# Kernel optimization log

Measured on AMD Instinct MI355X. Metric: run time of the kernel, lower is better.

Reference implementation:

```python
import jax, jax.numpy as jnp
import numpy as np

BINS = 64

def _soft_histogram(x, bins=BINS):
    # x: (B, C, H, W), values expected in [0, 1]
    B, C, H, W = x.shape
    x_flat = x.reshape(B, C, H * W)                       # (B, C, N)
    bin_width = 1.0 / bins
    centers = jnp.linspace(bin_width / 2, 1 - bin_width / 2, bins,
                           dtype=x.dtype)                 # (bins,)
    sigma = bin_width
    # weights: (B, C, N, bins) gaussian kernel around each bin center
    diff = x_flat[..., None] - centers                    # (B, C, N, bins)
    weights = jnp.exp(-(diff ** 2) / (2.0 * sigma ** 2))
    hist = weights.sum(axis=2)                            # (B, C, bins)
    hist = hist / (hist.sum(axis=-1, keepdims=True) + 1e-08)
    return hist


def setup_inputs() -> dict:
    key = jax.random.key(0)
    k1, k2 = jax.random.split(key)
    pred = jax.random.uniform(k1, (4, 3, 512, 512), dtype=jnp.float32)
    target = jax.random.uniform(k2, (4, 3, 512, 512), dtype=jnp.float32)
    return {"pred": pred, "target": target}


def reference(pred, target):
    pred_hist = _soft_histogram(pred)
    target_hist = _soft_histogram(target)
    pred_cdf = jnp.cumsum(pred_hist, axis=-1)
    target_cdf = jnp.cumsum(target_hist, axis=-1)
    return jnp.mean(jnp.abs(pred_cdf - target_cdf))
```

## Files before the change

### kernel.cpp

```cpp
#include <hip/hip_runtime.h>
#include <stdint.h>

#define BINS    64
#define SBINS   256
#define CSTR    66
#define THREADS 128
#define CHUNKS  32
#define NPIX    (512*512)
#define PPB     (NPIX / CHUNKS)
#define ITERS   (PPB / 4 / THREADS)
#define NCH     12
#define NIMG    (2 * NCH)

__global__ __launch_bounds__(THREADS) void hist_kernel(
    const float* __restrict__ pred, const float* __restrict__ target,
    uint32_t* __restrict__ part ,
    uint32_t* __restrict__ ticket)
{
    __shared__ uint32_t lh[THREADS * CSTR];
    __shared__ uint32_t red[2 * THREADS];
    const int tid = threadIdx.x;

    if (blockIdx.x == 0 && blockIdx.y == 0 && blockIdx.z == 0 && tid == 0)
        *ticket = 0u;

    uint32_t* col = &lh[tid * CSTR];
    uint2* colv = (uint2*)col;
    #pragma unroll
    for (int i = 0; i < CSTR / 2; ++i) colv[i] = make_uint2(0u, 0u);
    __syncthreads();

    const int chunk = blockIdx.x;
    const int ch    = blockIdx.y;
    const int z     = blockIdx.z;
    const float* src = (z == 0 ? pred : target)
                     + (size_t)ch * NPIX + (size_t)chunk * PPB;
    const float4* src4 = (const float4*)src;

    float4 v0 = src4[tid];
    float4 v1 = src4[THREADS + tid];
    #pragma unroll
    for (int k = 0; k < ITERS; ++k) {
        float4 v2 = (k + 2 < ITERS) ? src4[(size_t)(k + 2) * THREADS + tid]
                                    : make_float4(0.f, 0.f, 0.f, 0.f);
        float xv[4] = {v0.x, v0.y, v0.z, v0.w};
        #pragma unroll
        for (int e = 0; e < 4; ++e) {
            uint32_t kq = (uint32_t)(int)(xv[e] * 256.0f);
            col[kq >> 2] += 1u << ((kq & 3u) << 3);
        }
        v0 = v1; v1 = v2;
    }
    __syncthreads();

    const int d = tid & 63;
    const int g = tid >> 6;
    uint32_t lo = 0u, hi = 0u;
    #pragma unroll 8
    for (int c = 0; c < 64; ++c) {
        uint32_t x = lh[(g * 64 + c) * CSTR + d];
        lo += x & 0x00FF00FFu;
        hi += (x >> 8) & 0x00FF00FFu;
    }
    red[tid] = lo;
    red[THREADS + tid] = hi;
    __syncthreads();

    if (tid < 64) {
        uint32_t tlo = red[tid] + red[tid + 64];
        uint32_t thi = red[THREADS + tid] + red[THREADS + tid + 64];
        uint4 o;
        o.x = tlo & 0xFFFFu;
        o.y = thi & 0xFFFFu;
        o.z = tlo >> 16;
        o.w = thi >> 16;
        uint4* pp = (uint4*)(part + (((size_t)z * NCH + ch) * CHUNKS + chunk) * SBINS);
        pp[tid] = o;
    }
}

__global__ __launch_bounds__(SBINS) void conv_fin_kernel(
    const uint32_t* __restrict__ part, float* __restrict__ partial,
    uint32_t* __restrict__ ticket, float* __restrict__ out)
{
    __shared__ float cntP[SBINS], cntT[SBINS];
    __shared__ float histP[BINS], histT[BINS];
    const int ci = blockIdx.x;
    const int s  = threadIdx.x;

    uint32_t tp = 0u, tt = 0u;
    #pragma unroll 8
    for (int i = 0; i < CHUNKS; ++i) {
        tp += part[((size_t)ci * CHUNKS + i) * SBINS + s];
        tt += part[((size_t)(NCH + ci) * CHUNKS + i) * SBINS + s];
    }
    cntP[s] = (float)tp;
    cntT[s] = (float)tt;
    __syncthreads();

    if (s < 2 * BINS) {
        const int b = s & 63;
        const float* cnt = (s < BINS) ? cntP : cntT;
        float h = 0.0f;
        #pragma unroll
        for (int u = -16; u <= 19; ++u) {
            int idx = 4 * b + u;
            if (idx >= 0 && idx < SBINS) {
                float t = (u - 1.5f) * 0.25f;
                h += __expf(-0.5f * t * t) * cnt[idx];
            }
        }
        if (s < BINS) histP[b] = h; else histT[b] = h;
    }
    __syncthreads();

    if (s < 64) {
        float cp = histP[s], ct = histT[s];
        #pragma unroll
        for (int off = 1; off < 64; off <<= 1) {
            float a = __shfl_up(cp, off, 64);
            float b = __shfl_up(ct, off, 64);
            if (s >= off) { cp += a; ct += b; }
        }
        float sp = __shfl(cp, 63, 64);
        float st = __shfl(ct, 63, 64);
        float diff = fabsf(cp / (sp + 1e-8f) - ct / (st + 1e-8f));
        #pragma unroll
        for (int off = 32; off; off >>= 1)
            diff += __shfl_xor(diff, off, 64);
        if (s == 0) {
            partial[ci] = diff;
            __threadfence();
            uint32_t old = atomicAdd(ticket, 1u);
            if (old == NCH - 1) {
                __threadfence();
                float acc = 0.0f;
                #pragma unroll
                for (int i = 0; i < NCH; ++i) acc += partial[i];
                out[0] = acc / (float)(NCH * BINS);
            }
        }
    }
}

extern "C" void kernel_launch(void* const* d_in, const int* in_sizes, int n_in,
                              void* d_out, int out_size, void* d_ws, size_t ws_size,
                              hipStream_t stream)
{
    const float* pred   = (const float*)d_in[0];
    const float* target = (const float*)d_in[1];
    uint32_t* part    = (uint32_t*)d_ws;
    float*    partial = (float*)(part + (size_t)NIMG * CHUNKS * SBINS);
    uint32_t* ticket  = (uint32_t*)(partial + NCH);

    hist_kernel<<<dim3(CHUNKS, NCH, 2), THREADS, 0, stream>>>(pred, target, part, ticket);
    conv_fin_kernel<<<NCH, SBINS, 0, stream>>>(part, partial, ticket, (float*)d_out);
}
```

Measured before the change: 17.32 us.

## Fuse histogram and finalize kernels via per-channel last-block tickets

Merges the convolution/finalize kernel into the histogram kernel. Each block increments a per-channel atomic ticket, and the last arriving block for a channel reduces all chunk partials, applies the Gaussian smoothing, and computes that channel's CDF difference. A global ticket then produces the final mean. Partial counts are packed as two 16-bit values per word, which halves the partial-buffer traffic. The goal is to remove the second kernel launch and its dependency gap, at the cost of a memset call and serialized tail work in the last block of each channel.

```diff
diff --git a/kernel.cpp b/kernel.cpp
--- a/kernel.cpp
+++ b/kernel.cpp
@@ -11,18 +11,27 @@
 #define ITERS   (PPB / 4 / THREADS)
 #define NCH     12
 #define NIMG    (2 * NCH)
+#define ARRIV   (CHUNKS * 2)
+#define PPW     128
 
-__global__ __launch_bounds__(THREADS) void hist_kernel(
+__device__ __forceinline__ uint32_t cload(const uint32_t* p) {
+    return __hip_atomic_load(p, __ATOMIC_RELAXED, __HIP_MEMORY_SCOPE_AGENT);
+}
+__device__ __forceinline__ void cstore(uint32_t* p, uint32_t v) {
+    __hip_atomic_store(p, v, __ATOMIC_RELAXED, __HIP_MEMORY_SCOPE_AGENT);
+}
+
+__global__ __launch_bounds__(THREADS) void fused_kernel(
     const float* __restrict__ pred, const float* __restrict__ target,
     uint32_t* __restrict__ part ,
-    uint32_t* __restrict__ ticket)
+    uint32_t* __restrict__ tickets ,
+    uint32_t* __restrict__ partial ,
+    float* __restrict__ out)
 {
     __shared__ uint32_t lh[THREADS * CSTR];
     __shared__ uint32_t red[2 * THREADS];
+    __shared__ uint32_t lastflag;
     const int tid = threadIdx.x;
-
-    if (blockIdx.x == 0 && blockIdx.y == 0 && blockIdx.z == 0 && tid == 0)
-        *ticket = 0u;
 
     uint32_t* col = &lh[tid * CSTR];
     uint2* colv = (uint2*)col;
@@ -69,38 +78,68 @@
     if (tid < 64) {
         uint32_t tlo = red[tid] + red[tid + 64];
         uint32_t thi = red[THREADS + tid] + red[THREADS + tid + 64];
-        uint4 o;
-        o.x = tlo & 0xFFFFu;
-        o.y = thi & 0xFFFFu;
-        o.z = tlo >> 16;
-        o.w = thi >> 16;
-        uint4* pp = (uint4*)(part + (((size_t)z * NCH + ch) * CHUNKS + chunk) * SBINS);
-        pp[tid] = o;
+        uint32_t w0 = (tlo & 0xFFFFu) | ((thi & 0xFFFFu) << 16);
+        uint32_t w1 = (tlo >> 16) | ((thi >> 16) << 16);
+        uint32_t* pp = part + (((size_t)z * NCH + ch) * CHUNKS + chunk) * PPW + 2 * d;
+        cstore(pp + 0, w0);
+        cstore(pp + 1, w1);
     }
-}
-
-__global__ __launch_bounds__(SBINS) void conv_fin_kernel(
-    const uint32_t* __restrict__ part, float* __restrict__ partial,
-    uint32_t* __restrict__ ticket, float* __restrict__ out)
-{
-    __shared__ float cntP[SBINS], cntT[SBINS];
-    __shared__ float histP[BINS], histT[BINS];
-    const int ci = blockIdx.x;
-    const int s  = threadIdx.x;
-
-    uint32_t tp = 0u, tt = 0u;
-    #pragma unroll 8
-    for (int i = 0; i < CHUNKS; ++i) {
-        tp += part[((size_t)ci * CHUNKS + i) * SBINS + s];
-        tt += part[((size_t)(NCH + ci) * CHUNKS + i) * SBINS + s];
-    }
-    cntP[s] = (float)tp;
-    cntT[s] = (float)tt;
     __syncthreads();
 
-    if (s < 2 * BINS) {
-        const int b = s & 63;
-        const float* cnt = (s < BINS) ? cntP : cntT;
+    if (tid == 0) {
+        uint32_t old = __hip_atomic_fetch_add(&tickets[ch], 1u,
+                          __ATOMIC_ACQ_REL, __HIP_MEMORY_SCOPE_AGENT);
+        lastflag = (old == ARRIV - 1u) ? 1u : 0u;
+    }
+    __syncthreads();
+    if (!lastflag) return;
+
+    uint32_t sP0 = 0u, sP1 = 0u, sT0 = 0u, sT1 = 0u;
+    {
+        const uint32_t* baseP = part + ((size_t)(0 * NCH + ch) * CHUNKS) * PPW + tid;
+        const uint32_t* baseT = part + ((size_t)(1 * NCH + ch) * CHUNKS) * PPW + tid;
+        #pragma unroll
+        for (int i = 0; i < CHUNKS; i += 8) {
+            uint32_t a0 = cload(baseP + (size_t)(i + 0) * PPW);
+            uint32_t a1 = cload(baseP + (size_t)(i + 1) * PPW);
+            uint32_t a2 = cload(baseP + (size_t)(i + 2) * PPW);
+            uint32_t a3 = cload(baseP + (size_t)(i + 3) * PPW);
+            uint32_t a4 = cload(baseP + (size_t)(i + 4) * PPW);
+            uint32_t a5 = cload(baseP + (size_t)(i + 5) * PPW);
+            uint32_t a6 = cload(baseP + (size_t)(i + 6) * PPW);
+            uint32_t a7 = cload(baseP + (size_t)(i + 7) * PPW);
+            uint32_t b0 = cload(baseT + (size_t)(i + 0) * PPW);
+            uint32_t b1 = cload(baseT + (size_t)(i + 1) * PPW);
+            uint32_t b2 = cload(baseT + (size_t)(i + 2) * PPW);
+            uint32_t b3 = cload(baseT + (size_t)(i + 3) * PPW);
+            uint32_t b4 = cload(baseT + (size_t)(i + 4) * PPW);
+            uint32_t b5 = cload(baseT + (size_t)(i + 5) * PPW);
+            uint32_t b6 = cload(baseT + (size_t)(i + 6) * PPW);
+            uint32_t b7 = cload(baseT + (size_t)(i + 7) * PPW);
+            sP0 += (a0 & 0xFFFFu) + (a1 & 0xFFFFu) + (a2 & 0xFFFFu) + (a3 & 0xFFFFu)
+                 + (a4 & 0xFFFFu) + (a5 & 0xFFFFu) + (a6 & 0xFFFFu) + (a7 & 0xFFFFu);
+            sP1 += (a0 >> 16) + (a1 >> 16) + (a2 >> 16) + (a3 >> 16)
+                 + (a4 >> 16) + (a5 >> 16) + (a6 >> 16) + (a7 >> 16);
+            sT0 += (b0 & 0xFFFFu) + (b1 & 0xFFFFu) + (b2 & 0xFFFFu) + (b3 & 0xFFFFu)
+                 + (b4 & 0xFFFFu) + (b5 & 0xFFFFu) + (b6 & 0xFFFFu) + (b7 & 0xFFFFu);
+            sT1 += (b0 >> 16) + (b1 >> 16) + (b2 >> 16) + (b3 >> 16)
+                 + (b4 >> 16) + (b5 >> 16) + (b6 >> 16) + (b7 >> 16);
+        }
+    }
+    __syncthreads();
+    float* cntP  = (float*)lh;
+    float* cntT  = cntP + SBINS;
+    float* histP = cntT + SBINS;
+    float* histT = histP + BINS;
+    cntP[2 * tid]     = (float)sP0;
+    cntP[2 * tid + 1] = (float)sP1;
+    cntT[2 * tid]     = (float)sT0;
+    cntT[2 * tid + 1] = (float)sT1;
+    __syncthreads();
+
+    {
+        const int b = tid & 63;
+        const float* cnt = (tid < 64) ? cntP : cntT;
         float h = 0.0f;
         #pragma unroll
         for (int u = -16; u <= 19; ++u) {
@@ -110,17 +149,17 @@
                 h += __expf(-0.5f * t * t) * cnt[idx];
             }
         }
-        if (s < BINS) histP[b] = h; else histT[b] = h;
+        if (tid < 64) histP[b] = h; else histT[b] = h;
     }
     __syncthreads();
 
-    if (s < 64) {
-        float cp = histP[s], ct = histT[s];
+    if (tid < 64) {
+        float cp = histP[tid], ct = histT[tid];
         #pragma unroll
         for (int off = 1; off < 64; off <<= 1) {
             float a = __shfl_up(cp, off, 64);
             float b = __shfl_up(ct, off, 64);
-            if (s >= off) { cp += a; ct += b; }
+            if (tid >= off) { cp += a; ct += b; }
         }
         float sp = __shfl(cp, 63, 64);
         float st = __shfl(ct, 63, 64);
@@ -128,15 +167,15 @@
         #pragma unroll
         for (int off = 32; off; off >>= 1)
             diff += __shfl_xor(diff, off, 64);
-        if (s == 0) {
-            partial[ci] = diff;
-            __threadfence();
-            uint32_t old = atomicAdd(ticket, 1u);
-            if (old == NCH - 1) {
-                __threadfence();
+        if (tid == 0) {
+            cstore(&partial[ch], __float_as_uint(diff));
+            uint32_t old = __hip_atomic_fetch_add(&tickets[NCH], 1u,
+                              __ATOMIC_ACQ_REL, __HIP_MEMORY_SCOPE_AGENT);
+            if (old == (uint32_t)(NCH - 1)) {
                 float acc = 0.0f;
                 #pragma unroll
-                for (int i = 0; i < NCH; ++i) acc += partial[i];
+                for (int i = 0; i < NCH; ++i)
+                    acc += __uint_as_float(cload(&partial[i]));
                 out[0] = acc / (float)(NCH * BINS);
             }
         }
@@ -150,9 +189,10 @@
     const float* pred   = (const float*)d_in[0];
     const float* target = (const float*)d_in[1];
     uint32_t* part    = (uint32_t*)d_ws;
-    float*    partial = (float*)(part + (size_t)NIMG * CHUNKS * SBINS);
-    uint32_t* ticket  = (uint32_t*)(partial + NCH);
+    uint32_t* tickets = part + (size_t)NIMG * CHUNKS * PPW;
+    uint32_t* partial = tickets + NCH + 1;
 
-    hist_kernel<<<dim3(CHUNKS, NCH, 2), THREADS, 0, stream>>>(pred, target, part, ticket);
-    conv_fin_kernel<<<NCH, SBINS, 0, stream>>>(part, partial, ticket, (float*)d_out);
+    hipMemsetAsync(tickets, 0, (NCH + 1) * sizeof(uint32_t), stream);
+    fused_kernel<<<dim3(CHUNKS, NCH, 2), THREADS, 0, stream>>>(
+        pred, target, part, tickets, partial, (float*)d_out);
 }
```

Measured after the change: 35.72 us. 106% more time.
